# Optimization experiments

Measured on AMD Instinct MI355X. Metric: run time of the kernel, lower is better.

## Reference

```python
import jax, jax.numpy as jnp
import numpy as np

TAU = 0.11
ALPHA = 32.0  # scale
EPS = 1e-12   # torch F.normalize eps


def _l2norm(t):
    n = jnp.linalg.norm(t, axis=-1, keepdims=True)
    return t / jnp.maximum(n, EPS)


def setup_inputs() -> dict:
    key = jax.random.key(0)
    k1, k2, k3, k4 = jax.random.split(key, 4)
    B, N, C, D = 8192, 100000, 1000, 768
    return {
        "x": jax.random.normal(k1, (B, D), dtype=jnp.float32),
        "support_features": jax.random.normal(k2, (N, D), dtype=jnp.float32),
        "support_labels": jax.random.randint(k3, (N,), 0, C),
        "W": jax.random.normal(k4, (D, D), dtype=jnp.float32) * 0.02,
        "b": jnp.zeros((D,), dtype=jnp.float32),
        "num_classes": C,
    }


def reference(x, support_features, support_labels, W, b, num_classes):
    def adapter(t):
        h = t @ W.T + b              # nn.Linear(D, D)
        return jax.nn.silu(h) + t    # SiLU + residual (use_zifa)

    embeddings = _l2norm(adapter(x))                      # (B, D)
    support_key = _l2norm(adapter(support_features))      # (N, D)

    # per-class mean prototype via one segment-sum pass
    sums = jax.ops.segment_sum(support_key, support_labels, num_segments=num_classes)  # (C, D)
    counts = jax.ops.segment_sum(
        jnp.ones((support_key.shape[0],), dtype=support_key.dtype),
        support_labels, num_segments=num_classes)          # (C,)
    means = sums / jnp.maximum(counts, 1.0)[:, None]
    prototypes = jnp.where((counts > 0)[:, None], _l2norm(means), 0.0)  # (C, D)

    # mvrec logits: exp(-(alpha - alpha*cos)) / tau
    cos_sim = embeddings @ prototypes.T                    # (B, C)
    logits = jnp.exp(-(ALPHA - ALPHA * cos_sim)) / max(TAU, 1e-9)
    predicts = jax.nn.softmax(logits, axis=-1)
    return predicts, logits, embeddings
```

## Files before the change

### kernel.cpp

```cpp
#include <hip/hip_runtime.h>
#include <hip/hip_bf16.h>
#include <stdint.h>

typedef __bf16 v8bf __attribute__((ext_vector_type(8)));
typedef float  v4f  __attribute__((ext_vector_type(4)));
typedef unsigned short u16;
typedef unsigned int   u32;

#define B_ROWS   8192
#define N_SUP    100000
#define N_CLS    1000
#define DIM      768
#define CPAD     1024
#define MSUP_PAD 100352

__device__ __forceinline__ u16 f2bf(float f) {
    union { float f; u32 u; } v; v.f = f;
    u32 r = 0x7FFFu + ((v.u >> 16) & 1u);
    return (u16)((v.u + r) >> 16);
}
__device__ __forceinline__ float bf2f(u16 b) {
    union { u32 u; float f; } v; v.u = ((u32)b) << 16; return v.f;
}
__device__ __forceinline__ u32 f2bf2(float lo, float hi) {
    __hip_bfloat162 h = __float22bfloat162_rn(make_float2(lo, hi));
    u32 u; __builtin_memcpy(&u, &h, 4); return u;
}
__device__ __forceinline__ void glds16(const void* g, void* l) {
    __builtin_amdgcn_global_load_lds((const __attribute__((address_space(1))) u32*)g,
                                     (__attribute__((address_space(3))) u32*)l, 16, 0, 0);
}

__device__ __forceinline__ float block_sum(float v, float* red) {
    #pragma unroll
    for (int o = 32; o > 0; o >>= 1) v += __shfl_down(v, o);
    int wv = threadIdx.x >> 6, ln = threadIdx.x & 63;
    if (ln == 0) red[wv] = v;
    __syncthreads();
    return red[0] + red[1] + red[2] + red[3];
}
__device__ __forceinline__ float block_max(float v, float* red) {
    #pragma unroll
    for (int o = 32; o > 0; o >>= 1) v = fmaxf(v, __shfl_down(v, o));
    int wv = threadIdx.x >> 6, ln = threadIdx.x & 63;
    if (ln == 0) red[wv] = v;
    __syncthreads();
    return fmaxf(fmaxf(red[0], red[1]), fmaxf(red[2], red[3]));
}

__global__ void conv_w_kernel(const float* __restrict__ in, u16* __restrict__ out) {
    size_t base = (size_t)blockIdx.x * DIM + threadIdx.x * 4;
    float4 v = *(const float4*)(in + base);
    ushort4 o;
    o.x = f2bf(v.x); o.y = f2bf(v.y); o.z = f2bf(v.z); o.w = f2bf(v.w);
    *(ushort4*)(out + base) = o;
}

template<bool BF16OUT>
__global__ __launch_bounds__(256)
void adapter_gemm_kernel(const float* __restrict__ A, const u16* __restrict__ Wb,
                         const float* __restrict__ bias,
                         u16* __restrict__ out_bf, float* __restrict__ out_f,
                         float* __restrict__ ss, int Mreal) {
    __shared__ u16 As[128 * 64];
    __shared__ u16 Bs[128 * 64];

    const int tid  = threadIdx.x;
    const int wave = tid >> 6, lane = tid & 63;
    const int fq = lane >> 4, fr = lane & 15;
    const int blk_m = blockIdx.y * 128, blk_n = blockIdx.x * 128;
    const int wm = (wave & 1) * 64, wn = (wave >> 1) * 64;

    v4f acc[4][4];
    #pragma unroll
    for (int i = 0; i < 4; i++)
        #pragma unroll
        for (int j = 0; j < 4; j++) acc[i][j] = (v4f){0.f, 0.f, 0.f, 0.f};

    const int rb = lane >> 3;
    const int cb = (lane & 7) * 8;
    const u16* gB = Wb + (size_t)(blk_n + wave * 8 + rb) * DIM + cb;

    for (int k0 = 0; k0 < DIM; k0 += 64) {
        #pragma unroll
        for (int p = 0; p < 4; p++)
            glds16(gB + (size_t)p * 32 * DIM + k0, Bs + p * 2048 + wave * 512);
        #pragma unroll
        for (int p = 0; p < 8; p++) {
            int idx = tid + p * 256;
            int row = idx >> 4;
            int c4  = (idx & 15) << 2;
            int gr  = blk_m + row; if (gr >= Mreal) gr = Mreal - 1;
            float4 v = *(const float4*)(A + (size_t)gr * DIM + k0 + c4);
            *(uint2*)(As + row * 64 + c4) = make_uint2(f2bf2(v.x, v.y), f2bf2(v.z, v.w));
        }
        __syncthreads();
        #pragma unroll
        for (int ks = 0; ks < 2; ks++) {
            const int kk = ks * 32;
            v8bf af[4], bfr[4];
            #pragma unroll
            for (int i = 0; i < 4; i++) {
                af[i]  = *(const v8bf*)(As + (wm + i * 16 + fr) * 64 + kk + fq * 8);
                bfr[i] = *(const v8bf*)(Bs + (wn + i * 16 + fr) * 64 + kk + fq * 8);
            }
            #pragma unroll
            for (int i = 0; i < 4; i++)
                #pragma unroll
                for (int j = 0; j < 4; j++)
                    acc[i][j] = __builtin_amdgcn_mfma_f32_16x16x32_bf16(
                        af[i], bfr[j], acc[i][j], 0, 0, 0);
        }
        __syncthreads();
    }

    #pragma unroll
    for (int i = 0; i < 4; i++) {
        int r0 = blk_m + wm + i * 16 + fq * 4;
        float ssp[4] = {0.f, 0.f, 0.f, 0.f};
        #pragma unroll
        for (int j = 0; j < 4; j++) {
            int col = blk_n + wn + j * 16 + fr;
            float bv = bias[col];
            #pragma unroll
            for (int r2 = 0; r2 < 4; r2++) {
                int gr = r0 + r2;
                bool ok = gr < Mreal;
                float h = acc[i][j][r2] + bv;
                float t = ok ? A[(size_t)gr * DIM + col] : 0.f;
                float v = h / (1.f + __expf(-h)) + t;
                ssp[r2] += v * v;
                if (ok) {
                    if (BF16OUT) out_bf[(size_t)gr * DIM + col] = f2bf(v);
                    else         out_f[(size_t)gr * DIM + col] = v;
                }
            }
        }
        #pragma unroll
        for (int r2 = 0; r2 < 4; r2++) {
            float s = ssp[r2];
            s += __shfl_xor(s, 1); s += __shfl_xor(s, 2);
            s += __shfl_xor(s, 4); s += __shfl_xor(s, 8);
            int gr = r0 + r2;
            if (fr == 0 && gr < Mreal) atomicAdd(&ss[gr], s);
        }
    }
}

__global__ void norm_x_kernel(const float* __restrict__ val, const float* __restrict__ ss,
                              float* __restrict__ emb, u16* __restrict__ emb_bf) {
    int row = blockIdx.x;
    float sc = 1.f / fmaxf(sqrtf(ss[row]), 1e-12f);
    size_t b = (size_t)row * DIM + threadIdx.x * 4;
    float4 v = *(const float4*)(val + b);
    float4 o; o.x = v.x * sc; o.y = v.y * sc; o.z = v.z * sc; o.w = v.w * sc;
    *(float4*)(emb + b) = o;
    ushort4 ob; ob.x = f2bf(o.x); ob.y = f2bf(o.y); ob.z = f2bf(o.z); ob.w = f2bf(o.w);
    *(ushort4*)(emb_bf + b) = ob;
}

__global__ __launch_bounds__(256)
void proto_kernel(const u16* __restrict__ val_bf, const float* __restrict__ ss,
                  const int* __restrict__ labels, u16* __restrict__ proto_bf) {
    __shared__ int queue[256];
    __shared__ int qn;
    __shared__ float red[4];
    const int cls = blockIdx.x, tid = threadIdx.x;
    if (tid == 0) qn = 0;
    __syncthreads();
    for (int i4 = tid; i4 < N_SUP / 4; i4 += 256) {
        int4 L = *(const int4*)(labels + i4 * 4);
        if (L.x == cls) queue[atomicAdd(&qn, 1) & 255] = i4 * 4;
        if (L.y == cls) queue[atomicAdd(&qn, 1) & 255] = i4 * 4 + 1;
        if (L.z == cls) queue[atomicAdd(&qn, 1) & 255] = i4 * 4 + 2;
        if (L.w == cls) queue[atomicAdd(&qn, 1) & 255] = i4 * 4 + 3;
    }
    __syncthreads();
    const int n = qn < 256 ? qn : 256;
    float a0 = 0.f, a1 = 0.f, a2 = 0.f;
    for (int e = 0; e < n; e++) {
        int row = queue[e];
        float sc = 1.f / fmaxf(sqrtf(ss[row]), 1e-12f);
        const u16* vr = val_bf + (size_t)row * DIM;
        a0 += bf2f(vr[tid])       * sc;
        a1 += bf2f(vr[tid + 256]) * sc;
        a2 += bf2f(vr[tid + 512]) * sc;
    }
    float inv_cnt = 1.f / fmaxf((float)n, 1.f);
    float m0 = a0 * inv_cnt, m1 = a1 * inv_cnt, m2 = a2 * inv_cnt;
    float tot = block_sum(m0 * m0 + m1 * m1 + m2 * m2, red);
    float sc2 = (n > 0) ? 1.f / fmaxf(sqrtf(tot), 1e-12f) : 0.f;
    size_t b = (size_t)cls * DIM;
    proto_bf[b + tid]       = f2bf(m0 * sc2);
    proto_bf[b + tid + 256] = f2bf(m1 * sc2);
    proto_bf[b + tid + 512] = f2bf(m2 * sc2);
}

__global__ __launch_bounds__(256)
void cos_gemm_kernel(const u16* __restrict__ Ab, const u16* __restrict__ Pb,
                     float* __restrict__ logits) {
    __shared__ u16 As[128 * 64];
    __shared__ u16 Bs[128 * 64];
    const int tid  = threadIdx.x;
    const int wave = tid >> 6, lane = tid & 63;
    const int fq = lane >> 4, fr = lane & 15;
    const int blk_m = blockIdx.y * 128, blk_n = blockIdx.x * 128;
    const int wm = (wave & 1) * 64, wn = (wave >> 1) * 64;

    v4f acc[4][4];
    #pragma unroll
    for (int i = 0; i < 4; i++)
        #pragma unroll
        for (int j = 0; j < 4; j++) acc[i][j] = (v4f){0.f, 0.f, 0.f, 0.f};

    const int rb = lane >> 3;
    const int cb = (lane & 7) * 8;
    const u16* gA = Ab + (size_t)(blk_m + wave * 8 + rb) * DIM + cb;
    const u16* gB = Pb + (size_t)(blk_n + wave * 8 + rb) * DIM + cb;

    for (int k0 = 0; k0 < DIM; k0 += 64) {
        #pragma unroll
        for (int p = 0; p < 4; p++) {
            glds16(gA + (size_t)p * 32 * DIM + k0, As + p * 2048 + wave * 512);
            glds16(gB + (size_t)p * 32 * DIM + k0, Bs + p * 2048 + wave * 512);
        }
        __syncthreads();
        #pragma unroll
        for (int ks = 0; ks < 2; ks++) {
            const int kk = ks * 32;
            v8bf af[4], bfr[4];
            #pragma unroll
            for (int i = 0; i < 4; i++) {
                af[i]  = *(const v8bf*)(As + (wm + i * 16 + fr) * 64 + kk + fq * 8);
                bfr[i] = *(const v8bf*)(Bs + (wn + i * 16 + fr) * 64 + kk + fq * 8);
            }
            #pragma unroll
            for (int i = 0; i < 4; i++)
                #pragma unroll
                for (int j = 0; j < 4; j++)
                    acc[i][j] = __builtin_amdgcn_mfma_f32_16x16x32_bf16(
                        af[i], bfr[j], acc[i][j], 0, 0, 0);
        }
        __syncthreads();
    }

    #pragma unroll
    for (int i = 0; i < 4; i++) {
        int r0 = blk_m + wm + i * 16 + fq * 4;
        #pragma unroll
        for (int j = 0; j < 4; j++) {
            int col = blk_n + wn + j * 16 + fr;
            if (col < N_CLS) {
                #pragma unroll
                for (int r2 = 0; r2 < 4; r2++) {
                    float c = acc[i][j][r2];
                    logits[(size_t)(r0 + r2) * N_CLS + col] =
                        expf(32.0f * (c - 1.0f)) * (1.0f / 0.11f);
                }
            }
        }
    }
}

__global__ __launch_bounds__(256)
void softmax_kernel(const float* __restrict__ logits, float* __restrict__ predicts) {
    __shared__ float redm[4];
    __shared__ float reds[4];
    int row = blockIdx.x, tid = threadIdx.x;
    const float* lr = logits + (size_t)row * N_CLS;
    float4 lg = make_float4(-1.f, -1.f, -1.f, -1.f);
    bool act = tid < N_CLS / 4;
    if (act) lg = *(const float4*)(lr + tid * 4);
    float mx = fmaxf(fmaxf(lg.x, lg.y), fmaxf(lg.z, lg.w));
    float mxt = block_max(mx, redm);
    float4 e = make_float4(0.f, 0.f, 0.f, 0.f);
    float s = 0.f;
    if (act) {
        e.x = expf(lg.x - mxt); e.y = expf(lg.y - mxt);
        e.z = expf(lg.z - mxt); e.w = expf(lg.w - mxt);
        s = e.x + e.y + e.z + e.w;
    }
    float st = block_sum(s, reds);
    float inv = 1.f / st;
    if (act) {
        float4 o; o.x = e.x * inv; o.y = e.y * inv; o.z = e.z * inv; o.w = e.w * inv;
        *(float4*)(predicts + (size_t)row * N_CLS + tid * 4) = o;
    }
}

extern "C" void kernel_launch(void* const* d_in, const int* in_sizes, int n_in,
                              void* d_out, int out_size, void* d_ws, size_t ws_size,
                              hipStream_t stream) {
    const float* x      = (const float*)d_in[0];
    const float* sup    = (const float*)d_in[1];
    const int*   labels = (const int*)d_in[2];
    const float* W      = (const float*)d_in[3];
    const float* bias   = (const float*)d_in[4];

    float* predicts = (float*)d_out;
    float* logits   = predicts + (size_t)B_ROWS * N_CLS;
    float* emb      = logits + (size_t)B_ROWS * N_CLS;

    char* ws = (char*)d_ws;
    size_t off = 0;
    u16*   w_bf     = (u16*)(ws + off);   off += (size_t)DIM * DIM * 2;
    u16*   val_sup  = (u16*)(ws + off);   off += (size_t)MSUP_PAD * DIM * 2;
    float* val_x    = (float*)(ws + off); off += (size_t)B_ROWS * DIM * 4;
    u16*   emb_bf   = (u16*)(ws + off);   off += (size_t)B_ROWS * DIM * 2;
    u16*   proto_bf = (u16*)(ws + off);   off += (size_t)CPAD * DIM * 2;
    float* ss_sup   = (float*)(ws + off); off += (size_t)MSUP_PAD * 4;
    float* ss_x     = (float*)(ws + off); off += (size_t)B_ROWS * 4;

    hipMemsetAsync(ss_sup, 0, ((size_t)MSUP_PAD + B_ROWS) * 4, stream);

    conv_w_kernel<<<DIM, 192, 0, stream>>>(W, w_bf);

    adapter_gemm_kernel<false><<<dim3(DIM / 128, B_ROWS / 128), 256, 0, stream>>>(
        x, w_bf, bias, nullptr, val_x, ss_x, B_ROWS);
    norm_x_kernel<<<B_ROWS, 192, 0, stream>>>(val_x, ss_x, emb, emb_bf);

    adapter_gemm_kernel<true><<<dim3(DIM / 128, MSUP_PAD / 128), 256, 0, stream>>>(
        sup, w_bf, bias, val_sup, nullptr, ss_sup, N_SUP);
    proto_kernel<<<CPAD, 256, 0, stream>>>(val_sup, ss_sup, labels, proto_bf);

    cos_gemm_kernel<<<dim3(CPAD / 128, B_ROWS / 128), 256, 0, stream>>>(
        emb_bf, proto_bf, logits);
    softmax_kernel<<<B_ROWS, 256, 0, stream>>>(logits, predicts);
}
```

Baseline: 1.035 ms.

## Pre-convert activations to padded bf16 and load adapter A tiles via async LDS

Adds a conversion pass that casts x and support features to zero-padded bf16 buffers, so the adapter GEMM can stream A tiles with global_load_lds instead of converting fp32 in registers. The x-path intermediate is also stored as bf16 instead of fp32. Exp calls in the cos GEMM and softmax switch to fast __expf. The extra conversion pass adds a full read and write of the inputs. Using the bf16 residual term and bf16 intermediates lowers precision.

```diff
diff --git a/kernel.cpp b/kernel.cpp
--- a/kernel.cpp
+++ b/kernel.cpp
@@ -22,10 +22,6 @@
 __device__ __forceinline__ float bf2f(u16 b) {
     union { u32 u; float f; } v; v.u = ((u32)b) << 16; return v.f;
 }
-__device__ __forceinline__ u32 f2bf2(float lo, float hi) {
-    __hip_bfloat162 h = __float22bfloat162_rn(make_float2(lo, hi));
-    u32 u; __builtin_memcpy(&u, &h, 4); return u;
-}
 __device__ __forceinline__ void glds16(const void* g, void* l) {
     __builtin_amdgcn_global_load_lds((const __attribute__((address_space(1))) u32*)g,
                                      (__attribute__((address_space(3))) u32*)l, 16, 0, 0);
@@ -48,20 +44,24 @@
     return fmaxf(fmaxf(red[0], red[1]), fmaxf(red[2], red[3]));
 }
 
-__global__ void conv_w_kernel(const float* __restrict__ in, u16* __restrict__ out) {
-    size_t base = (size_t)blockIdx.x * DIM + threadIdx.x * 4;
-    float4 v = *(const float4*)(in + base);
+__global__ void conv_pad_kernel(const float* __restrict__ in, u16* __restrict__ out,
+                                int n_real) {
+    int r = blockIdx.x;
+    size_t ob = (size_t)r * DIM + threadIdx.x * 4;
     ushort4 o;
-    o.x = f2bf(v.x); o.y = f2bf(v.y); o.z = f2bf(v.z); o.w = f2bf(v.w);
-    *(ushort4*)(out + base) = o;
-}
-
-template<bool BF16OUT>
+    if (r < n_real) {
+        float4 v = *(const float4*)(in + ob);
+        o.x = f2bf(v.x); o.y = f2bf(v.y); o.z = f2bf(v.z); o.w = f2bf(v.w);
+    } else {
+        o.x = 0; o.y = 0; o.z = 0; o.w = 0;
+    }
+    *(ushort4*)(out + ob) = o;
+}
+
 __global__ __launch_bounds__(256)
-void adapter_gemm_kernel(const float* __restrict__ A, const u16* __restrict__ Wb,
+void adapter_gemm_kernel(const u16* __restrict__ A, const u16* __restrict__ Wb,
                          const float* __restrict__ bias,
-                         u16* __restrict__ out_bf, float* __restrict__ out_f,
-                         float* __restrict__ ss, int Mreal) {
+                         u16* __restrict__ val, float* __restrict__ ss) {
     __shared__ u16 As[128 * 64];
     __shared__ u16 Bs[128 * 64];
 
@@ -79,20 +79,14 @@
 
     const int rb = lane >> 3;
     const int cb = (lane & 7) * 8;
+    const u16* gA = A  + (size_t)(blk_m + wave * 8 + rb) * DIM + cb;
     const u16* gB = Wb + (size_t)(blk_n + wave * 8 + rb) * DIM + cb;
 
     for (int k0 = 0; k0 < DIM; k0 += 64) {
         #pragma unroll
-        for (int p = 0; p < 4; p++)
+        for (int p = 0; p < 4; p++) {
+            glds16(gA + (size_t)p * 32 * DIM + k0, As + p * 2048 + wave * 512);
             glds16(gB + (size_t)p * 32 * DIM + k0, Bs + p * 2048 + wave * 512);
-        #pragma unroll
-        for (int p = 0; p < 8; p++) {
-            int idx = tid + p * 256;
-            int row = idx >> 4;
-            int c4  = (idx & 15) << 2;
-            int gr  = blk_m + row; if (gr >= Mreal) gr = Mreal - 1;
-            float4 v = *(const float4*)(A + (size_t)gr * DIM + k0 + c4);
-            *(uint2*)(As + row * 64 + c4) = make_uint2(f2bf2(v.x, v.y), f2bf2(v.z, v.w));
         }
         __syncthreads();
         #pragma unroll
@@ -125,15 +119,11 @@
             #pragma unroll
             for (int r2 = 0; r2 < 4; r2++) {
                 int gr = r0 + r2;
-                bool ok = gr < Mreal;
                 float h = acc[i][j][r2] + bv;
-                float t = ok ? A[(size_t)gr * DIM + col] : 0.f;
+                float t = bf2f(A[(size_t)gr * DIM + col]);
                 float v = h / (1.f + __expf(-h)) + t;
                 ssp[r2] += v * v;
-                if (ok) {
-                    if (BF16OUT) out_bf[(size_t)gr * DIM + col] = f2bf(v);
-                    else         out_f[(size_t)gr * DIM + col] = v;
-                }
+                val[(size_t)gr * DIM + col] = f2bf(v);
             }
         }
         #pragma unroll
@@ -141,19 +131,20 @@
             float s = ssp[r2];
             s += __shfl_xor(s, 1); s += __shfl_xor(s, 2);
             s += __shfl_xor(s, 4); s += __shfl_xor(s, 8);
-            int gr = r0 + r2;
-            if (fr == 0 && gr < Mreal) atomicAdd(&ss[gr], s);
-        }
-    }
-}
-
-__global__ void norm_x_kernel(const float* __restrict__ val, const float* __restrict__ ss,
+            if (fr == 0) atomicAdd(&ss[r0 + r2], s);
+        }
+    }
+}
+
+__global__ void norm_x_kernel(const u16* __restrict__ val, const float* __restrict__ ss,
                               float* __restrict__ emb, u16* __restrict__ emb_bf) {
     int row = blockIdx.x;
     float sc = 1.f / fmaxf(sqrtf(ss[row]), 1e-12f);
     size_t b = (size_t)row * DIM + threadIdx.x * 4;
-    float4 v = *(const float4*)(val + b);
-    float4 o; o.x = v.x * sc; o.y = v.y * sc; o.z = v.z * sc; o.w = v.w * sc;
+    ushort4 v = *(const ushort4*)(val + b);
+    float4 o;
+    o.x = bf2f(v.x) * sc; o.y = bf2f(v.y) * sc;
+    o.z = bf2f(v.z) * sc; o.w = bf2f(v.w) * sc;
     *(float4*)(emb + b) = o;
     ushort4 ob; ob.x = f2bf(o.x); ob.y = f2bf(o.y); ob.z = f2bf(o.z); ob.w = f2bf(o.w);
     *(ushort4*)(emb_bf + b) = ob;
@@ -255,7 +246,7 @@
                 for (int r2 = 0; r2 < 4; r2++) {
                     float c = acc[i][j][r2];
                     logits[(size_t)(r0 + r2) * N_CLS + col] =
-                        expf(32.0f * (c - 1.0f)) * (1.0f / 0.11f);
+                        __expf(32.0f * (c - 1.0f)) * (1.0f / 0.11f);
                 }
             }
         }
@@ -276,8 +267,8 @@
     float4 e = make_float4(0.f, 0.f, 0.f, 0.f);
     float s = 0.f;
     if (act) {
-        e.x = expf(lg.x - mxt); e.y = expf(lg.y - mxt);
-        e.z = expf(lg.z - mxt); e.w = expf(lg.w - mxt);
+        e.x = __expf(lg.x - mxt); e.y = __expf(lg.y - mxt);
+        e.z = __expf(lg.z - mxt); e.w = __expf(lg.w - mxt);
         s = e.x + e.y + e.z + e.w;
     }
     float st = block_sum(s, reds);
@@ -304,8 +295,10 @@
     char* ws = (char*)d_ws;
     size_t off = 0;
     u16*   w_bf     = (u16*)(ws + off);   off += (size_t)DIM * DIM * 2;
+    u16*   x_bf     = (u16*)(ws + off);   off += (size_t)B_ROWS * DIM * 2;
+    u16*   sup_bf   = (u16*)(ws + off);   off += (size_t)MSUP_PAD * DIM * 2;
+    u16*   val_x    = (u16*)(ws + off);   off += (size_t)B_ROWS * DIM * 2;
     u16*   val_sup  = (u16*)(ws + off);   off += (size_t)MSUP_PAD * DIM * 2;
-    float* val_x    = (float*)(ws + off); off += (size_t)B_ROWS * DIM * 4;
     u16*   emb_bf   = (u16*)(ws + off);   off += (size_t)B_ROWS * DIM * 2;
     u16*   proto_bf = (u16*)(ws + off);   off += (size_t)CPAD * DIM * 2;
     float* ss_sup   = (float*)(ws + off); off += (size_t)MSUP_PAD * 4;
@@ -313,14 +306,17 @@
 
     hipMemsetAsync(ss_sup, 0, ((size_t)MSUP_PAD + B_ROWS) * 4, stream);
 
-    conv_w_kernel<<<DIM, 192, 0, stream>>>(W, w_bf);
-
-    adapter_gemm_kernel<false><<<dim3(DIM / 128, B_ROWS / 128), 256, 0, stream>>>(
-        x, w_bf, bias, nullptr, val_x, ss_x, B_ROWS);
+    conv_pad_kernel<<<DIM,      192, 0, stream>>>(W,   w_bf,   DIM);
+    conv_pad_kernel<<<B_ROWS,   192, 0, stream>>>(x,   x_bf,   B_ROWS);
+    conv_pad_kernel<<<MSUP_PAD, 192, 0, stream>>>(sup, sup_bf, N_SUP);
+
+    adapter_gemm_kernel<<<dim3(DIM / 128, B_ROWS / 128), 256, 0, stream>>>(
+        x_bf, w_bf, bias, val_x, ss_x);
+    adapter_gemm_kernel<<<dim3(DIM / 128, MSUP_PAD / 128), 256, 0, stream>>>(
+        sup_bf, w_bf, bias, val_sup, ss_sup);
+
     norm_x_kernel<<<B_ROWS, 192, 0, stream>>>(val_x, ss_x, emb, emb_bf);
 
-    adapter_gemm_kernel<true><<<dim3(DIM / 128, MSUP_PAD / 128), 256, 0, stream>>>(
-        sup, w_bf, bias, val_sup, nullptr, ss_sup, N_SUP);
     proto_kernel<<<CPAD, 256, 0, stream>>>(val_sup, ss_sup, labels, proto_bf);
 
     cos_gemm_kernel<<<dim3(CPAD / 128, B_ROWS / 128), 256, 0, stream>>>(
```

Result: faster. 915.2 us (-11.6%).
